# Kernel tuning notes

Measured on AMD Instinct MI355X. Metric: run time of the kernel, lower is better.

Reference implementation:

```python
import jax, jax.numpy as jnp
import numpy as np

B, GRID, D, NF, NC = 4096, 8, 64, 256, 10
N = GRID * GRID          # num_nodes = grid_size**2
LN_EPS = 1e-5            # torch LayerNorm default eps


def _grid_mask():
    m = np.zeros((N, N), np.float32)
    for i in range(N):
        r, c = divmod(i, GRID)
        if r > 0: m[i, i - GRID] = 1
        if r < GRID - 1: m[i, i + GRID] = 1
        if c > 0: m[i, i - 1] = 1
        if c < GRID - 1: m[i, i + 1] = 1
    return jnp.asarray(m)

MASK = _grid_mask()  # static 4-neighbor grid adjacency mask [N,N]


def _ln(x, g, b):
    mu = x.mean(-1, keepdims=True)
    v = ((x - mu) ** 2).mean(-1, keepdims=True)  # biased var, like torch LayerNorm
    return (x - mu) / jnp.sqrt(v + LN_EPS) * g + b


def _regulator(x, h_pre, w_norm, p):
    # HomeostaticRegulator.forward (eval mode: baselines fixed at 0.5 / 1.0)
    var = jnp.var(x, axis=1, ddof=1, keepdims=True)            # torch.var default unbiased=True
    natural_stress = jnp.abs(var - 0.5)
    xs = jnp.sort(x, axis=1)
    smoothness = jnp.abs(xs[:, 1:] - xs[:, :-1]).mean(1, keepdims=True)
    adversarial_stress = jnp.abs(smoothness - 1.0)
    excitation = jnp.abs(h_pre).mean(1, keepdims=True)
    fatigue = jnp.broadcast_to(jnp.reshape(w_norm, (1, 1)), (x.shape[0], 1))
    gradient_proxy = jnp.sqrt((h_pre ** 2).mean(1, keepdims=True))
    s = jnp.concatenate([natural_stress, adversarial_stress, excitation, fatigue, gradient_proxy], axis=1)
    h = jnp.tanh(_ln(s @ p[0].T + p[1], p[2], p[3]))
    h = jnp.tanh(_ln(h @ p[4].T + p[5], p[6], p[7]))
    return jax.nn.sigmoid(h @ p[8].T + p[9])  # [B,3] = metabolism, sensitivity, gate


def _cell(x, W_slow, W_fast, ln_g, ln_b, cp):
    # HomeoContinuumCell.forward, eval mode (no Hebbian buffer update)
    h_raw = jax.lax.stop_gradient(x @ W_slow.T)                 # computed under torch.no_grad
    w_norm = jax.lax.stop_gradient(jnp.sqrt((W_slow ** 2).sum()))
    ctl = _regulator(x, h_raw, w_norm, cp)
    beta = 0.5 + ctl[:, 1:2] * 2.0
    gate = ctl[:, 2:3]
    comb = x @ W_slow.T + (x @ W_fast.T) * gate
    act = comb * jax.nn.sigmoid(beta * comb)
    return _ln(act, ln_g, ln_b)


def _forward(x, W_embed, b_embed, adj_weights, W_slow, W_fast, ln_g, ln_b, W_read, b_read, tp, cp):
    e = x @ W_embed.T + b_embed                                 # [B, N*D]
    e3 = e.reshape(B, N, D)
    # HomeoTopology.get_adjacency with homeostasis (all under no_grad in torch)
    ts = jax.lax.stop_gradient(e.reshape(1, -1))                # flatten whole batch state
    wn = jax.lax.stop_gradient(jnp.sqrt((adj_weights ** 2).sum()))
    ctl = jax.lax.stop_gradient(_regulator(ts, ts, wn, tp))
    ap = ctl[:, 0].mean()                                       # plasticity(=1.0) * mean metabolism
    adj = jax.nn.sigmoid(adj_weights * ap) * MASK
    adj = adj / jnp.clip(adj.sum(1, keepdims=True), 1e-6, None)
    m = jnp.einsum('nm,bmd->bnd', adj, e3)                      # grid message passing
    proc = _cell(m.reshape(B * N, D), W_slow, W_fast, ln_g, ln_b, cp)
    return proc.reshape(B, N * D) @ W_read.T + b_read           # logits [B, NC]


def _reg_params(key, scale=0.2):
    ks = jax.random.split(key, 3)
    return (jax.random.normal(ks[0], (16, 5)) * scale, jnp.zeros(16), jnp.ones(16), jnp.zeros(16),
            jax.random.normal(ks[1], (8, 16)) * scale, jnp.zeros(8), jnp.ones(8), jnp.zeros(8),
            jax.random.normal(ks[2], (3, 8)) * scale, jnp.zeros(3))


def setup_inputs() -> dict:
    key = jax.random.key(0)
    ks = jax.random.split(key, 9)
    inp = {
        'x': jax.random.normal(ks[0], (B, NF)),
        'W_embed': jax.random.normal(ks[1], (N * D, NF)) * (1.0 / np.sqrt(NF)),
        'b_embed': jnp.zeros(N * D),
        'adj_weights': jax.random.normal(ks[2], (N, N)) * 0.1,
        'W_slow': jax.random.normal(ks[3], (D, D)) * (1.4 / np.sqrt(D)),
        'W_fast': jax.random.normal(ks[4], (D, D)) * 0.05,
        'ln_g': jnp.ones(D), 'ln_b': jnp.zeros(D),
        'W_read': jax.random.normal(ks[5], (NC, N * D)) * (1.0 / np.sqrt(N * D)),
        'b_read': jnp.zeros(NC),
    }
    names = ['W1', 'b1', 'g1', 'bb1', 'W2', 'b2', 'g2', 'bb2', 'W3', 'b3']
    for pre, k in (('t', ks[6]), ('c', ks[7])):
        for n, v in zip(names, _reg_params(k)):
            inp[pre + '_' + n] = v
    return inp


def reference(x, W_embed, b_embed, adj_weights, W_slow, W_fast, ln_g, ln_b, W_read, b_read,
              t_W1, t_b1, t_g1, t_bb1, t_W2, t_b2, t_g2, t_bb2, t_W3, t_b3,
              c_W1, c_b1, c_g1, c_bb1, c_W2, c_b2, c_g2, c_bb2, c_W3, c_b3):
    tp = (t_W1, t_b1, t_g1, t_bb1, t_W2, t_b2, t_g2, t_bb2, t_W3, t_b3)
    cp = (c_W1, c_b1, c_g1, c_bb1, c_W2, c_b2, c_g2, c_bb2, c_W3, c_b3)
    return _forward(x, W_embed, b_embed, adj_weights, W_slow, W_fast, ln_g, ln_b, W_read, b_read, tp, cp)
```

## Files before the change

kernel.cpp:

```cpp
#include <hip/hip_runtime.h>

typedef unsigned short u16;
typedef unsigned int   u32;
typedef float f32x4 __attribute__((ext_vector_type(4)));
typedef int   i32x4 __attribute__((ext_vector_type(4)));
typedef int   i32x2 __attribute__((ext_vector_type(2)));
typedef short s8v   __attribute__((ext_vector_type(8)));

__device__ inline u16 f2bf(float f) {
  u32 u = __float_as_uint(f);
  return (u16)((u + 0x7FFFu + ((u >> 16) & 1u)) >> 16);
}
__device__ inline float bf2f(u16 h) { return __uint_as_float(((u32)h) << 16); }
__device__ inline float bflo(int u) { return __uint_as_float(((u32)u) << 16); }
__device__ inline float bfhi(int u) { return __uint_as_float(((u32)u) & 0xFFFF0000u); }

__device__ inline u32 fkey(float f) {
  u32 u = __float_as_uint(f);
  return (u & 0x80000000u) ? ~u : (u | 0x80000000u);
}
__device__ inline float unkey(u32 k) {
  u32 u = (k & 0x80000000u) ? (k & 0x7FFFFFFFu) : ~k;
  return __uint_as_float(u);
}
__device__ inline float fast_tanh(float x) {
  float cx = fminf(fmaxf(x, -15.f), 15.f);
  float e = __expf(2.f * cx);
  return __fdividef(e - 1.f, e + 1.f);
}
__device__ inline float sigm(float x) { return __fdividef(1.f, 1.f + __expf(-x)); }

__device__ inline void gload_lds16(const u16* g, u16* l) {
  __builtin_amdgcn_global_load_lds((const __attribute__((address_space(1))) u32*)g,
                                   (__attribute__((address_space(3))) u32*)l, 16, 0, 0);
}

struct MlpP { const float *W1,*b1,*g1,*bb1,*W2,*b2,*g2,*bb2,*W3,*b3; };

__device__ inline void mlp_eval(const MlpP& p, const float* s, float* ctl) {
  float h1[16];
  float mu = 0.f;
  #pragma unroll
  for (int i = 0; i < 16; ++i) {
    float v = p.b1[i];
    #pragma unroll
    for (int k = 0; k < 5; ++k) v = fmaf(p.W1[i*5+k], s[k], v);
    h1[i] = v; mu += v;
  }
  mu *= (1.0f/16.0f);
  float vv = 0.f;
  #pragma unroll
  for (int i = 0; i < 16; ++i) { float d = h1[i]-mu; vv += d*d; }
  vv *= (1.0f/16.0f);
  float inv = 1.0f/sqrtf(vv + 1e-5f);
  #pragma unroll
  for (int i = 0; i < 16; ++i) h1[i] = fast_tanh((h1[i]-mu)*inv*p.g1[i] + p.bb1[i]);
  float h2[8];
  mu = 0.f;
  #pragma unroll
  for (int o = 0; o < 8; ++o) {
    float v = p.b2[o];
    #pragma unroll
    for (int i = 0; i < 16; ++i) v = fmaf(p.W2[o*16+i], h1[i], v);
    h2[o] = v; mu += v;
  }
  mu *= 0.125f;
  vv = 0.f;
  #pragma unroll
  for (int o = 0; o < 8; ++o) { float d = h2[o]-mu; vv += d*d; }
  vv *= 0.125f;
  inv = 1.0f/sqrtf(vv + 1e-5f);
  #pragma unroll
  for (int o = 0; o < 8; ++o) h2[o] = fast_tanh((h2[o]-mu)*inv*p.g2[o] + p.bb2[o]);
  #pragma unroll
  for (int c = 0; c < 3; ++c) {
    float v = p.b3[c];
    #pragma unroll
    for (int o = 0; o < 8; ++o) v = fmaf(p.W3[c*8+o], h2[o], v);
    ctl[c] = sigm(v);
  }
}

__global__ __launch_bounds__(256) void k_cast(const float* __restrict__ in,
                                              u16* __restrict__ out, int n) {
  int i = (blockIdx.x * 256 + threadIdx.x) * 4;
  if (i < n) {
    f32x4 v = *(const f32x4*)(in + i);
    u16 o[4] = { f2bf(v[0]), f2bf(v[1]), f2bf(v[2]), f2bf(v[3]) };
    *(u32*)(out + i)     = ((u32)o[1] << 16) | o[0];
    *(u32*)(out + i + 2) = ((u32)o[3] << 16) | o[2];
  }
}

__global__ void k_init(float* S) {
  int t = threadIdx.x;
  if (t < 3) S[t] = 0.f;
  if (t == 3) ((u32*)S)[3] = 0xFFFFFFFFu;
  if (t == 4) ((u32*)S)[4] = 0u;
}

__global__ __launch_bounds__(256) void k_gemm(const u16* __restrict__ Xb,
                                              const u16* __restrict__ Wb,
                                              const float* __restrict__ bias,
                                              u16* __restrict__ E,
                                              float* __restrict__ S) {
  __shared__ __align__(16) u16 As[128*64];
  __shared__ __align__(16) u16 Bs[128*64];
  const int t = threadIdx.x;
  const int wv = t >> 6, lane = t & 63;
  const int wr = wv >> 1, wc = wv & 1;
  const int i0 = blockIdx.y * 128, j0 = blockIdx.x * 128;
  const int rr = lane & 15, q = lane >> 4;
  const int lrow = lane >> 3, lcol = (lane & 7) * 8;
  f32x4 acc[4][4] = {};
  for (int k0 = 0; k0 < 256; k0 += 64) {
    #pragma unroll
    for (int r = 0; r < 4; ++r) {
      const int row = (r*4 + wv)*8 + lrow;
      gload_lds16(Xb + (size_t)(i0 + row)*256 + k0 + lcol, &As[(r*4 + wv)*512]);
      gload_lds16(Wb + (size_t)(j0 + row)*256 + k0 + lcol, &Bs[(r*4 + wv)*512]);
    }
    __syncthreads();
    #pragma unroll
    for (int ks = 0; ks < 2; ++ks) {
      s8v a[4], b[4];
      #pragma unroll
      for (int m = 0; m < 4; ++m) a[m] = *(const s8v*)&As[(wr*64 + m*16 + rr)*64 + ks*32 + q*8];
      #pragma unroll
      for (int n = 0; n < 4; ++n) b[n] = *(const s8v*)&Bs[(wc*64 + n*16 + rr)*64 + ks*32 + q*8];
      #pragma unroll
      for (int m = 0; m < 4; ++m)
        #pragma unroll
        for (int n = 0; n < 4; ++n)
          acc[m][n] = __builtin_amdgcn_mfma_f32_16x16x32_bf16(a[m], b[n], acc[m][n], 0, 0, 0);
    }
    __syncthreads();
  }
  float s = 0.f, ss = 0.f, sa = 0.f, mnv = 1e30f, mxv = -1e30f;
  #pragma unroll
  for (int n = 0; n < 4; ++n) {
    const int col = j0 + wc*64 + n*16 + rr;
    const float bv = bias[col];
    #pragma unroll
    for (int m = 0; m < 4; ++m) {
      const int rowb = i0 + wr*64 + m*16 + q*4;
      #pragma unroll
      for (int r = 0; r < 4; ++r) {
        float v = acc[m][n][r] + bv;
        E[(size_t)(rowb + r)*4096 + col] = f2bf(v);
        s += v; ss = fmaf(v, v, ss); sa += fabsf(v);
        mnv = fminf(mnv, v); mxv = fmaxf(mxv, v);
      }
    }
  }
  #pragma unroll
  for (int off = 32; off; off >>= 1) {
    s += __shfl_xor(s, off); ss += __shfl_xor(ss, off); sa += __shfl_xor(sa, off);
    mnv = fminf(mnv, __shfl_xor(mnv, off));
    mxv = fmaxf(mxv, __shfl_xor(mxv, off));
  }
  __shared__ float red5[4][5];
  if (lane == 0) { red5[wv][0]=s; red5[wv][1]=ss; red5[wv][2]=sa; red5[wv][3]=mnv; red5[wv][4]=mxv; }
  __syncthreads();
  if (t == 0) {
    float S0 = red5[0][0]+red5[1][0]+red5[2][0]+red5[3][0];
    float S1 = red5[0][1]+red5[1][1]+red5[2][1]+red5[3][1];
    float S2 = red5[0][2]+red5[1][2]+red5[2][2]+red5[3][2];
    float Mn = fminf(fminf(red5[0][3],red5[1][3]), fminf(red5[2][3],red5[3][3]));
    float Mx = fmaxf(fmaxf(red5[0][4],red5[1][4]), fmaxf(red5[2][4],red5[3][4]));
    atomicAdd(&S[0], S0); atomicAdd(&S[1], S1); atomicAdd(&S[2], S2);
    atomicMin((u32*)S + 3, fkey(Mn));
    atomicMax((u32*)S + 4, fkey(Mx));
  }
}

__global__ __launch_bounds__(256) void k_prep(const float* __restrict__ adjw,
    const float* __restrict__ Wslow,
    const float* tW1, const float* tb1, const float* tg1, const float* tbb1,
    const float* tW2, const float* tb2, const float* tg2, const float* tbb2,
    const float* tW3, const float* tb3,
    float* __restrict__ S) {
  __shared__ float red[2][256];
  __shared__ float apL;
  const int t = threadIdx.x;
  float a = 0.f, w = 0.f;
  for (int i = t; i < 4096; i += 256) {
    float v = adjw[i]; a = fmaf(v, v, a);
    float u = Wslow[i]; w = fmaf(u, u, w);
  }
  red[0][t] = a; red[1][t] = w;
  __syncthreads();
  for (int sred = 128; sred > 0; sred >>= 1) {
    if (t < sred) { red[0][t] += red[0][t+sred]; red[1][t] += red[1][t+sred]; }
    __syncthreads();
  }
  if (t == 0) {
    float wn_t = sqrtf(red[0][0]);
    float wn_c = sqrtf(red[1][0]);
    S[7] = wn_c;
    const float n = 16777216.0f, n1 = 16777215.0f;
    float sum = S[0], sumsq = S[1], sumabs = S[2];
    float mean = sum / n;
    float var = (sumsq - sum*mean) / n1;
    float mn = unkey(((u32*)S)[3]);
    float mx = unkey(((u32*)S)[4]);
    float sfv[5];
    sfv[0] = fabsf(var - 0.5f);
    sfv[1] = fabsf((mx - mn)/n1 - 1.0f);
    sfv[2] = sumabs / n;
    sfv[3] = wn_t;
    sfv[4] = sqrtf(sumsq / n);
    MlpP p{tW1,tb1,tg1,tbb1,tW2,tb2,tg2,tbb2,tW3,tb3};
    float ctl[3];
    mlp_eval(p, sfv, ctl);
    apL = ctl[0];
    S[6] = ctl[0];
  }
  __syncthreads();
  if (t < 64) {
    const int rr = t >> 3, cc = t & 7;
    const float ap = apL;
    const int nb[4] = { rr>0 ? t-8 : -1, rr<7 ? t+8 : -1, cc>0 ? t-1 : -1, cc<7 ? t+1 : -1 };
    float w4[4]; float rs = 0.f;
    #pragma unroll
    for (int qq = 0; qq < 4; ++qq) {
      w4[qq] = (nb[qq] >= 0) ? sigm(adjw[t*64 + nb[qq]] * ap) : 0.0f;
      rs += w4[qq];
    }
    rs = fmaxf(rs, 1e-6f);
    #pragma unroll
    for (int qq = 0; qq < 4; ++qq) S[8 + t*4 + qq] = w4[qq] / rs;
  }
}

__global__ __launch_bounds__(256) void k_cell(const u16* __restrict__ E,
    const float* __restrict__ Ws, const float* __restrict__ Wf,
    const float* __restrict__ lng, const float* __restrict__ lnb,
    const float* __restrict__ Wread, const float* __restrict__ bread,
    const float* __restrict__ S,
    const float* cW1, const float* cb1, const float* cg1, const float* cbb1,
    const float* cW2, const float* cb2, const float* cg2, const float* cbb2,
    const float* cW3, const float* cb3,
    float* __restrict__ out) {
  __shared__ __align__(16) u16 ebh[64][72];
  __shared__ __align__(16) u16 mh[64][72];
  __shared__ __align__(16) u16 WsH[64][72];
  __shared__ __align__(16) u16 WfH[64][72];
  __shared__ __align__(16) float adjcL[256];
  __shared__ __align__(16) float prm[308];
  __shared__ __align__(16) float lngL[64], lnbL[64];
  __shared__ float wavp[4][10];
  __shared__ float wncL;

  const int t = threadIdx.x;
  const int wv = t >> 6, lane = t & 63;
  const int b = blockIdx.x;
  const u16* Eb = E + (size_t)b * 4096;

  #pragma unroll
  for (int r = 0; r < 2; ++r) {
    int c = t + r*256;
    int n = c >> 3, d8 = (c & 7) * 8;
    *(i32x4*)&ebh[n][d8] = *(const i32x4*)(Eb + n*64 + d8);
  }
  #pragma unroll
  for (int r = 0; r < 4; ++r) {
    int c = t + r*256;
    int n = c >> 4, d = (c & 15) * 4;
    f32x4 vs = *(const f32x4*)(Ws + c*4);
    f32x4 vf = *(const f32x4*)(Wf + c*4);
    i32x2 ps = { (int)((((u32)f2bf(vs[1]))<<16) | f2bf(vs[0])),
                 (int)((((u32)f2bf(vs[3]))<<16) | f2bf(vs[2])) };
    i32x2 pf = { (int)((((u32)f2bf(vf[1]))<<16) | f2bf(vf[0])),
                 (int)((((u32)f2bf(vf[3]))<<16) | f2bf(vf[2])) };
    *(i32x2*)&WsH[n][d] = ps;
    *(i32x2*)&WfH[n][d] = pf;
  }
  adjcL[t] = S[8 + t];
  for (int i = t; i < 80;  i += 256) prm[i] = cW1[i];
  if (t < 16) { prm[80+t]=cb1[t]; prm[96+t]=cg1[t]; prm[112+t]=cbb1[t]; }
  for (int i = t; i < 128; i += 256) prm[128+i] = cW2[i];
  if (t < 8)  { prm[256+t]=cb2[t]; prm[264+t]=cg2[t]; prm[272+t]=cbb2[t]; }
  if (t < 24) prm[280+t] = cW3[t];
  if (t < 3)  prm[304+t] = cb3[t];
  if (t < 64) { lngL[t] = lng[t]; lnbL[t] = lnb[t]; }
  if (t == 0) wncL = S[7];
  __syncthreads();

  {
    const int d = lane;
    #pragma unroll
    for (int i = 0; i < 16; ++i) {
      const int n = wv*16 + i;
      const int gr = n >> 3, gc = n & 7;
      const int nb0 = gr > 0 ? n - 8 : 0;
      const int nb1 = gr < 7 ? n + 8 : 0;
      const int nb2 = gc > 0 ? n - 1 : 0;
      const int nb3 = gc < 7 ? n + 1 : 0;
      float acc = adjcL[n*4+0]*bf2f(ebh[nb0][d]) + adjcL[n*4+1]*bf2f(ebh[nb1][d])
                + adjcL[n*4+2]*bf2f(ebh[nb2][d]) + adjcL[n*4+3]*bf2f(ebh[nb3][d]);
      mh[n][d] = f2bf(acc);
    }
  }
  __syncthreads();

  const int rr = lane & 15, q = lane >> 4;
  const int n = wv*16 + rr;
  s8v bm0 = *(const s8v*)&mh[n][q*8];
  s8v bm1 = *(const s8v*)&mh[n][32 + q*8];
  f32x4 hs[4], hf[4];
  #pragma unroll
  for (int jt = 0; jt < 4; ++jt) {
    const u16* wsr = &WsH[jt*16 + rr][0];
    const u16* wfr = &WfH[jt*16 + rr][0];
    s8v aw0 = *(const s8v*)(wsr + q*8), aw1 = *(const s8v*)(wsr + 32 + q*8);
    s8v af0 = *(const s8v*)(wfr + q*8), af1 = *(const s8v*)(wfr + 32 + q*8);
    f32x4 z = {0.f, 0.f, 0.f, 0.f};
    hs[jt] = __builtin_amdgcn_mfma_f32_16x16x32_bf16(aw0, bm0, z, 0, 0, 0);
    hs[jt] = __builtin_amdgcn_mfma_f32_16x16x32_bf16(aw1, bm1, hs[jt], 0, 0, 0);
    hf[jt] = __builtin_amdgcn_mfma_f32_16x16x32_bf16(af0, bm0, z, 0, 0, 0);
    hf[jt] = __builtin_amdgcn_mfma_f32_16x16x32_bf16(af1, bm1, hf[jt], 0, 0, 0);
  }

  float s1 = 0.f, s2 = 0.f, mnv = 1e30f, mxv = -1e30f;
  #pragma unroll
  for (int j = 0; j < 8; ++j) {
    float v0 = bf2f((u16)bm0[j]), v1 = bf2f((u16)bm1[j]);
    s1 += v0 + v1;
    s2 = fmaf(v0, v0, s2); s2 = fmaf(v1, v1, s2);
    mnv = fminf(mnv, fminf(v0, v1));
    mxv = fmaxf(mxv, fmaxf(v0, v1));
  }
  float sa = 0.f, sq = 0.f;
  #pragma unroll
  for (int jt = 0; jt < 4; ++jt)
    #pragma unroll
    for (int r = 0; r < 4; ++r) { float v = hs[jt][r]; sa += fabsf(v); sq = fmaf(v, v, sq); }
  #pragma unroll
  for (int off = 16; off <= 32; off <<= 1) {
    s1 += __shfl_xor(s1, off); s2 += __shfl_xor(s2, off);
    sa += __shfl_xor(sa, off); sq += __shfl_xor(sq, off);
    mnv = fminf(mnv, __shfl_xor(mnv, off));
    mxv = fmaxf(mxv, __shfl_xor(mxv, off));
  }
  float var = (s2 - s1*s1*(1.f/64.f)) * (1.f/63.f);
  float sfv[5];
  sfv[0] = fabsf(var - 0.5f);
  sfv[1] = fabsf((mxv - mnv)*(1.f/63.f) - 1.f);
  sfv[2] = sa * (1.f/64.f);
  sfv[3] = wncL;
  sfv[4] = sqrtf(sq * (1.f/64.f));
  MlpP p{prm, prm+80, prm+96, prm+112, prm+128, prm+256, prm+264, prm+272, prm+280, prm+304};
  float ctl[3];
  mlp_eval(p, sfv, ctl);
  const float beta = 0.5f + 2.f*ctl[1], gate = ctl[2];

  float acts[4][4];
  float a1 = 0.f, a2 = 0.f;
  #pragma unroll
  for (int jt = 0; jt < 4; ++jt)
    #pragma unroll
    for (int r = 0; r < 4; ++r) {
      float comb = fmaf(hf[jt][r], gate, hs[jt][r]);
      float sv = comb * sigm(beta * comb);
      acts[jt][r] = sv;
      a1 += sv; a2 = fmaf(sv, sv, a2);
    }
  a1 += __shfl_xor(a1, 16); a2 += __shfl_xor(a2, 16);
  a1 += __shfl_xor(a1, 32); a2 += __shfl_xor(a2, 32);
  float mu = a1 * (1.f/64.f);
  float vvv = a2 * (1.f/64.f) - mu*mu;
  float inv = 1.f / sqrtf(vvv + 1e-5f);
  float racc[10];
  #pragma unroll
  for (int c = 0; c < 10; ++c) racc[c] = 0.f;
  #pragma unroll
  for (int jt = 0; jt < 4; ++jt) {
    f32x4 gv = *(const f32x4*)&lngL[jt*16 + q*4];
    f32x4 bv = *(const f32x4*)&lnbL[jt*16 + q*4];
    float pr[4];
    #pragma unroll
    for (int r = 0; r < 4; ++r) pr[r] = (acts[jt][r] - mu)*inv*gv[r] + bv[r];
    const float* wrb = Wread + n*64 + jt*16 + q*4;
    #pragma unroll
    for (int c = 0; c < 10; ++c) {
      f32x4 w = *(const f32x4*)(wrb + c*4096);
      racc[c] += pr[0]*w[0] + pr[1]*w[1] + pr[2]*w[2] + pr[3]*w[3];
    }
  }
  #pragma unroll
  for (int c = 0; c < 10; ++c) {
    float v = racc[c];
    #pragma unroll
    for (int off = 1; off < 64; off <<= 1) v += __shfl_xor(v, off);
    if (lane == 0) wavp[wv][c] = v;
  }
  __syncthreads();
  if (t < 10) out[(size_t)b*10 + t] = bread[t] + wavp[0][t] + wavp[1][t] + wavp[2][t] + wavp[3][t];
}

extern "C" void kernel_launch(void* const* d_in, const int* in_sizes, int n_in,
                              void* d_out, int out_size, void* d_ws, size_t ws_size,
                              hipStream_t stream) {
  (void)in_sizes; (void)n_in; (void)out_size; (void)ws_size;
  const float* x       = (const float*)d_in[0];
  const float* W_embed = (const float*)d_in[1];
  const float* b_embed = (const float*)d_in[2];
  const float* adjw    = (const float*)d_in[3];
  const float* Wslow   = (const float*)d_in[4];
  const float* Wfast   = (const float*)d_in[5];
  const float* lng     = (const float*)d_in[6];
  const float* lnb     = (const float*)d_in[7];
  const float* Wread   = (const float*)d_in[8];
  const float* bread   = (const float*)d_in[9];
  float* out = (float*)d_out;

  char* ws = (char*)d_ws;
  u16*   Ebf = (u16*)ws;
  u16*   Xbf = (u16*)(ws + 33554432);
  u16*   Wbf = (u16*)(ws + 35651584);
  float* S   = (float*)(ws + 37748736);

  hipLaunchKernelGGL(k_cast, dim3(1024), dim3(256), 0, stream, x, Xbf, 1048576);
  hipLaunchKernelGGL(k_cast, dim3(1024), dim3(256), 0, stream, W_embed, Wbf, 1048576);
  hipLaunchKernelGGL(k_init, dim3(1), dim3(64), 0, stream, S);
  hipLaunchKernelGGL(k_gemm, dim3(32, 32), dim3(256), 0, stream, Xbf, Wbf, b_embed, Ebf, S);
  hipLaunchKernelGGL(k_prep, dim3(1), dim3(256), 0, stream, adjw, Wslow,
                     (const float*)d_in[10], (const float*)d_in[11], (const float*)d_in[12], (const float*)d_in[13],
                     (const float*)d_in[14], (const float*)d_in[15], (const float*)d_in[16], (const float*)d_in[17],
                     (const float*)d_in[18], (const float*)d_in[19], S);
  hipLaunchKernelGGL(k_cell, dim3(4096), dim3(256), 0, stream, Ebf, Wslow, Wfast, lng, lnb,
                     Wread, bread, S,
                     (const float*)d_in[20], (const float*)d_in[21], (const float*)d_in[22], (const float*)d_in[23],
                     (const float*)d_in[24], (const float*)d_in[25], (const float*)d_in[26], (const float*)d_in[27],
                     (const float*)d_in[28], (const float*)d_in[29], out);
}
```

Baseline: 332.8 us.

## Fuse cast kernels, precast cell weights, cut LDS and dedupe per-node MLP

Merges the two bf16 cast kernels and the init kernel into one launch, which also converts W_slow and W_fast to bf16 once so each cell block loads them directly instead of reconverting. The cell kernel reuses one LDS buffer for the embedding, the message result and the scratch arrays, and adds a launch bound asking for five blocks per SM, aiming at higher occupancy. The regulator MLP now runs once per node on 64 threads, with results shared through LDS, instead of redundantly in every lane. The price is extra __syncthreads barriers and possible register pressure or spills under the tighter launch bound.

```diff
diff --git a/kernel.cpp b/kernel.cpp
--- a/kernel.cpp
+++ b/kernel.cpp
@@ -12,8 +12,6 @@
   return (u16)((u + 0x7FFFu + ((u >> 16) & 1u)) >> 16);
 }
 __device__ inline float bf2f(u16 h) { return __uint_as_float(((u32)h) << 16); }
-__device__ inline float bflo(int u) { return __uint_as_float(((u32)u) << 16); }
-__device__ inline float bfhi(int u) { return __uint_as_float(((u32)u) & 0xFFFF0000u); }
 
 __device__ inline u32 fkey(float f) {
   u32 u = __float_as_uint(f);
@@ -81,22 +79,42 @@
   }
 }
 
-__global__ __launch_bounds__(256) void k_cast(const float* __restrict__ in,
-                                              u16* __restrict__ out, int n) {
-  int i = (blockIdx.x * 256 + threadIdx.x) * 4;
-  if (i < n) {
-    f32x4 v = *(const f32x4*)(in + i);
+__global__ __launch_bounds__(256) void k_pre(const float* __restrict__ x,
+                                             const float* __restrict__ We,
+                                             const float* __restrict__ Ws,
+                                             const float* __restrict__ Wf,
+                                             u16* __restrict__ Xb, u16* __restrict__ Wb,
+                                             u16* __restrict__ WsB, u16* __restrict__ WfB,
+                                             float* __restrict__ S) {
+  const int bi = blockIdx.x, t = threadIdx.x;
+  if (bi < 2048) {
+    const float* src = (bi < 1024) ? x : We;
+    u16* dst = (bi < 1024) ? Xb : Wb;
+    int i = ((bi & 1023) * 256 + t) * 4;
+    f32x4 v = *(const f32x4*)(src + i);
     u16 o[4] = { f2bf(v[0]), f2bf(v[1]), f2bf(v[2]), f2bf(v[3]) };
-    *(u32*)(out + i)     = ((u32)o[1] << 16) | o[0];
-    *(u32*)(out + i + 2) = ((u32)o[3] << 16) | o[2];
-  }
-}
-
-__global__ void k_init(float* S) {
-  int t = threadIdx.x;
-  if (t < 3) S[t] = 0.f;
-  if (t == 3) ((u32*)S)[3] = 0xFFFFFFFFu;
-  if (t == 4) ((u32*)S)[4] = 0u;
+    *(u32*)(dst + i)     = ((u32)o[1] << 16) | o[0];
+    *(u32*)(dst + i + 2) = ((u32)o[3] << 16) | o[2];
+  } else {
+    #pragma unroll
+    for (int m = 0; m < 2; ++m) {
+      const float* src = m ? Wf : Ws;
+      u16* dst = m ? WfB : WsB;
+      int base = t * 16;
+      u16 o[16];
+      #pragma unroll
+      for (int r = 0; r < 4; ++r) {
+        f32x4 v = *(const f32x4*)(src + base + r*4);
+        o[r*4+0]=f2bf(v[0]); o[r*4+1]=f2bf(v[1]); o[r*4+2]=f2bf(v[2]); o[r*4+3]=f2bf(v[3]);
+      }
+      #pragma unroll
+      for (int r = 0; r < 8; ++r)
+        *(u32*)(dst + base + r*2) = ((u32)o[r*2+1] << 16) | o[r*2];
+    }
+    if (t < 3) S[t] = 0.f;
+    if (t == 3) ((u32*)S)[3] = 0xFFFFFFFFu;
+    if (t == 4) ((u32*)S)[4] = 0u;
+  }
 }
 
 __global__ __launch_bounds__(256) void k_gemm(const u16* __restrict__ Xb,
@@ -233,8 +251,8 @@
   }
 }
 
-__global__ __launch_bounds__(256) void k_cell(const u16* __restrict__ E,
-    const float* __restrict__ Ws, const float* __restrict__ Wf,
+__global__ __launch_bounds__(256, 5) void k_cell(const u16* __restrict__ E,
+    const u16* __restrict__ WsB, const u16* __restrict__ WfB,
     const float* __restrict__ lng, const float* __restrict__ lnb,
     const float* __restrict__ Wread, const float* __restrict__ bread,
     const float* __restrict__ S,
@@ -242,39 +260,30 @@
     const float* cW2, const float* cb2, const float* cg2, const float* cbb2,
     const float* cW3, const float* cb3,
     float* __restrict__ out) {
-  __shared__ __align__(16) u16 ebh[64][72];
-  __shared__ __align__(16) u16 mh[64][72];
+  __shared__ __align__(16) u16 ebM[64][72];
   __shared__ __align__(16) u16 WsH[64][72];
   __shared__ __align__(16) u16 WfH[64][72];
   __shared__ __align__(16) float adjcL[256];
   __shared__ __align__(16) float prm[308];
   __shared__ __align__(16) float lngL[64], lnbL[64];
-  __shared__ float wavp[4][10];
   __shared__ float wncL;
+  float* const sfvL = (float*)&ebM[0][0];
+  float* const bgL  = (float*)&ebM[0][0] + 320;
+  float* const wavp = (float*)&ebM[0][0] + 448;
 
   const int t = threadIdx.x;
   const int wv = t >> 6, lane = t & 63;
   const int b = blockIdx.x;
   const u16* Eb = E + (size_t)b * 4096;
 
-  #pragma unroll
-  for (int r = 0; r < 2; ++r) {
-    int c = t + r*256;
-    int n = c >> 3, d8 = (c & 7) * 8;
-    *(i32x4*)&ebh[n][d8] = *(const i32x4*)(Eb + n*64 + d8);
-  }
-  #pragma unroll
-  for (int r = 0; r < 4; ++r) {
-    int c = t + r*256;
-    int n = c >> 4, d = (c & 15) * 4;
-    f32x4 vs = *(const f32x4*)(Ws + c*4);
-    f32x4 vf = *(const f32x4*)(Wf + c*4);
-    i32x2 ps = { (int)((((u32)f2bf(vs[1]))<<16) | f2bf(vs[0])),
-                 (int)((((u32)f2bf(vs[3]))<<16) | f2bf(vs[2])) };
-    i32x2 pf = { (int)((((u32)f2bf(vf[1]))<<16) | f2bf(vf[0])),
-                 (int)((((u32)f2bf(vf[3]))<<16) | f2bf(vf[2])) };
-    *(i32x2*)&WsH[n][d] = ps;
-    *(i32x2*)&WfH[n][d] = pf;
+  {
+    const int row = t >> 2, c16 = (t & 3) * 16;
+    *(i32x4*)&ebM[row][c16]     = *(const i32x4*)(Eb  + row*64 + c16);
+    *(i32x4*)&ebM[row][c16 + 8] = *(const i32x4*)(Eb  + row*64 + c16 + 8);
+    *(i32x4*)&WsH[row][c16]     = *(const i32x4*)(WsB + row*64 + c16);
+    *(i32x4*)&WsH[row][c16 + 8] = *(const i32x4*)(WsB + row*64 + c16 + 8);
+    *(i32x4*)&WfH[row][c16]     = *(const i32x4*)(WfB + row*64 + c16);
+    *(i32x4*)&WfH[row][c16 + 8] = *(const i32x4*)(WfB + row*64 + c16 + 8);
   }
   adjcL[t] = S[8 + t];
   for (int i = t; i < 80;  i += 256) prm[i] = cW1[i];
@@ -287,6 +296,7 @@
   if (t == 0) wncL = S[7];
   __syncthreads();
 
+  float macc[16];
   {
     const int d = lane;
     #pragma unroll
@@ -297,17 +307,19 @@
       const int nb1 = gr < 7 ? n + 8 : 0;
       const int nb2 = gc > 0 ? n - 1 : 0;
       const int nb3 = gc < 7 ? n + 1 : 0;
-      float acc = adjcL[n*4+0]*bf2f(ebh[nb0][d]) + adjcL[n*4+1]*bf2f(ebh[nb1][d])
-                + adjcL[n*4+2]*bf2f(ebh[nb2][d]) + adjcL[n*4+3]*bf2f(ebh[nb3][d]);
-      mh[n][d] = f2bf(acc);
-    }
-  }
+      macc[i] = adjcL[n*4+0]*bf2f(ebM[nb0][d]) + adjcL[n*4+1]*bf2f(ebM[nb1][d])
+              + adjcL[n*4+2]*bf2f(ebM[nb2][d]) + adjcL[n*4+3]*bf2f(ebM[nb3][d]);
+    }
+  }
+  __syncthreads();
+  #pragma unroll
+  for (int i = 0; i < 16; ++i) ebM[wv*16 + i][lane] = f2bf(macc[i]);
   __syncthreads();
 
   const int rr = lane & 15, q = lane >> 4;
   const int n = wv*16 + rr;
-  s8v bm0 = *(const s8v*)&mh[n][q*8];
-  s8v bm1 = *(const s8v*)&mh[n][32 + q*8];
+  s8v bm0 = *(const s8v*)&ebM[n][q*8];
+  s8v bm1 = *(const s8v*)&ebM[n][32 + q*8];
   f32x4 hs[4], hf[4];
   #pragma unroll
   for (int jt = 0; jt < 4; ++jt) {
@@ -343,18 +355,29 @@
     mnv = fminf(mnv, __shfl_xor(mnv, off));
     mxv = fmaxf(mxv, __shfl_xor(mxv, off));
   }
-  float var = (s2 - s1*s1*(1.f/64.f)) * (1.f/63.f);
-  float sfv[5];
-  sfv[0] = fabsf(var - 0.5f);
-  sfv[1] = fabsf((mxv - mnv)*(1.f/63.f) - 1.f);
-  sfv[2] = sa * (1.f/64.f);
-  sfv[3] = wncL;
-  sfv[4] = sqrtf(sq * (1.f/64.f));
-  MlpP p{prm, prm+80, prm+96, prm+112, prm+128, prm+256, prm+264, prm+272, prm+280, prm+304};
-  float ctl[3];
-  mlp_eval(p, sfv, ctl);
-  const float beta = 0.5f + 2.f*ctl[1], gate = ctl[2];
-
+  if (q == 0) {
+    float var = (s2 - s1*s1*(1.f/64.f)) * (1.f/63.f);
+    sfvL[n*5+0] = fabsf(var - 0.5f);
+    sfvL[n*5+1] = fabsf((mxv - mnv)*(1.f/63.f) - 1.f);
+    sfvL[n*5+2] = sa * (1.f/64.f);
+    sfvL[n*5+3] = wncL;
+    sfvL[n*5+4] = sqrtf(sq * (1.f/64.f));
+  }
+  __syncthreads();
+
+  if (t < 64) {
+    float sfv[5];
+    #pragma unroll
+    for (int k = 0; k < 5; ++k) sfv[k] = sfvL[t*5+k];
+    MlpP p{prm, prm+80, prm+96, prm+112, prm+128, prm+256, prm+264, prm+272, prm+280, prm+304};
+    float ctl[3];
+    mlp_eval(p, sfv, ctl);
+    bgL[t*2+0] = 0.5f + 2.f*ctl[1];
+    bgL[t*2+1] = ctl[2];
+  }
+  __syncthreads();
+
+  const float beta = bgL[n*2+0], gate = bgL[n*2+1];
   float acts[4][4];
   float a1 = 0.f, a2 = 0.f;
   #pragma unroll
@@ -393,10 +416,10 @@
     float v = racc[c];
     #pragma unroll
     for (int off = 1; off < 64; off <<= 1) v += __shfl_xor(v, off);
-    if (lane == 0) wavp[wv][c] = v;
-  }
-  __syncthreads();
-  if (t < 10) out[(size_t)b*10 + t] = bread[t] + wavp[0][t] + wavp[1][t] + wavp[2][t] + wavp[3][t];
+    if (lane == 0) wavp[wv*10 + c] = v;
+  }
+  __syncthreads();
+  if (t < 10) out[(size_t)b*10 + t] = bread[t] + wavp[0*10+t] + wavp[1*10+t] + wavp[2*10+t] + wavp[3*10+t];
 }
 
 extern "C" void kernel_launch(void* const* d_in, const int* in_sizes, int n_in,
@@ -416,20 +439,21 @@
   float* out = (float*)d_out;
 
   char* ws = (char*)d_ws;
-  u16*   Ebf = (u16*)ws;
-  u16*   Xbf = (u16*)(ws + 33554432);
-  u16*   Wbf = (u16*)(ws + 35651584);
-  float* S   = (float*)(ws + 37748736);
-
-  hipLaunchKernelGGL(k_cast, dim3(1024), dim3(256), 0, stream, x, Xbf, 1048576);
-  hipLaunchKernelGGL(k_cast, dim3(1024), dim3(256), 0, stream, W_embed, Wbf, 1048576);
-  hipLaunchKernelGGL(k_init, dim3(1), dim3(64), 0, stream, S);
+  u16*   Ebf  = (u16*)ws;
+  u16*   Xbf  = (u16*)(ws + 33554432);
+  u16*   Wbf  = (u16*)(ws + 35651584);
+  float* S    = (float*)(ws + 37748736);
+  u16*   WsBf = (u16*)(ws + 37752832);
+  u16*   WfBf = (u16*)(ws + 37761024);
+
+  hipLaunchKernelGGL(k_pre, dim3(2049), dim3(256), 0, stream,
+                     x, W_embed, Wslow, Wfast, Xbf, Wbf, WsBf, WfBf, S);
   hipLaunchKernelGGL(k_gemm, dim3(32, 32), dim3(256), 0, stream, Xbf, Wbf, b_embed, Ebf, S);
   hipLaunchKernelGGL(k_prep, dim3(1), dim3(256), 0, stream, adjw, Wslow,
                      (const float*)d_in[10], (const float*)d_in[11], (const float*)d_in[12], (const float*)d_in[13],
                      (const float*)d_in[14], (const float*)d_in[15], (const float*)d_in[16], (const float*)d_in[17],
                      (const float*)d_in[18], (const float*)d_in[19], S);
-  hipLaunchKernelGGL(k_cell, dim3(4096), dim3(256), 0, stream, Ebf, Wslow, Wfast, lng, lnb,
+  hipLaunchKernelGGL(k_cell, dim3(4096), dim3(256), 0, stream, Ebf, WsBf, WfBf, lng, lnb,
                      Wread, bread, S,
                      (const float*)d_in[20], (const float*)d_in[21], (const float*)d_in[22], (const float*)d_in[23],
                      (const float*)d_in[24], (const float*)d_in[25], (const float*)d_in[26], (const float*)d_in[27],
```

Result: slower. 367.6 us (+10.5%).
